# Optimization experiments

Measured on AMD Instinct MI355X. Metric: run time of the kernel, lower is better.

Reference implementation:

```python
import jax, jax.numpy as jnp
import numpy as np


def _binarize(x):
    # sign-binarization with straight-through estimator (matches torch .data trick)
    return x + jax.lax.stop_gradient(jnp.sign(x) - x)


def _conv(x, w):
    # x: NCHW, w: OIHW, stride 1, no padding (padding handled explicitly)
    return jax.lax.conv_general_dilated(
        x, w, window_strides=(1, 1), padding='VALID',
        dimension_numbers=('NCHW', 'OIHW', 'NCHW'))


def _hardtanh(x):
    return jnp.clip(x, -1.0, 1.0)


def _maxpool2(x):
    # 2x2 max pool, stride 2, over spatial dims of NCHW
    return jax.lax.reduce_window(
        x, -jnp.inf, jax.lax.max,
        window_dimensions=(1, 1, 2, 2), window_strides=(1, 1, 2, 2),
        padding='VALID')


def setup_inputs() -> dict:
    key = jax.random.key(0)
    kx, k1, k2, k3, k4 = jax.random.split(key, 5)
    x = jax.random.normal(kx, (32, 3, 512, 512), dtype=jnp.float32)
    w1 = jax.random.normal(k1, (8, 3, 3, 3), dtype=jnp.float32) * 0.1
    w2 = jax.random.normal(k2, (16, 8, 3, 3), dtype=jnp.float32) * 0.1
    w3 = jax.random.normal(k3, (32, 16, 3, 3), dtype=jnp.float32) * 0.1
    w4 = jax.random.normal(k4, (2, 32, 3, 3), dtype=jnp.float32) * 0.1
    return {'x': x, 'w1': w1, 'w2': w2, 'w3': w3, 'w4': w4}


def reference(x, w1, w2, w3, w4):
    # p0: ConstantPad2d(1, value=1)
    h = jnp.pad(x, ((0, 0), (0, 0), (1, 1), (1, 1)), constant_values=1.0)
    # features1: BinarizeConv2d(3,8) -- input has 3 channels so NOT binarized;
    # weights are sign-binarized. Then Hardtanh, MaxPool2d(2,2).
    h = _maxpool2(_hardtanh(_conv(h, _binarize(w1))))          # [B,8,256,256]
    # features2..4: binarize activations (C != 3) and weights, conv, hardtanh
    h = _hardtanh(_conv(_binarize(h), _binarize(w2)))          # [B,16,254,254]
    h = _hardtanh(_conv(_binarize(h), _binarize(w3)))          # [B,32,252,252]
    h = _hardtanh(_conv(_binarize(h), _binarize(w4)))          # [B,2,250,250]
    return h.reshape(h.shape[0], -1)                           # [B, 125000]
```

## Files before the change

### kernel.cpp

```cpp
#include <hip/hip_runtime.h>
#include <hip/hip_bf16.h>
#include <cstdint>


typedef __attribute__((ext_vector_type(2)))  float f32x2;
typedef __attribute__((ext_vector_type(4)))  int int4v;
typedef __attribute__((ext_vector_type(16))) int int16v;

#define WOFF_W2M 0
#define WOFF_W3M 10240
#define WOFF_W4P 20480
#define WOFF_W1D 28672
#define WEIGHTS_BYTES 32768

#define A1_PB (2*256*256*4)
#define A2_PB (4*254*254*4)

__device__ __forceinline__ int dot4(int a, int b, int c) {
#if __has_builtin(__builtin_amdgcn_sdot4)
    return __builtin_amdgcn_sdot4(a, b, c, false);
#else
    int s = c;
#pragma unroll
    for (int j = 0; j < 4; ++j) {
        int av = (a << (24 - 8 * j)) >> 24;
        int bv = (b << (24 - 8 * j)) >> 24;
        s += av * bv;
    }
    return s;
#endif
}

__device__ __forceinline__ int fsign(float w) {
    return (w > 0.f) ? 1 : ((w < 0.f) ? -1 : 0);
}

__device__ __forceinline__ void pkfma_lo(f32x2& acc, f32x2 w, f32x2 v) {
    asm("v_pk_fma_f32 %0, %1, %2, %0 op_sel:[0,0,0] op_sel_hi:[1,0,1]"
        : "+v"(acc) : "s"(w), "v"(v));
}
__device__ __forceinline__ void pkfma_hi(f32x2& acc, f32x2 w, f32x2 v) {
    asm("v_pk_fma_f32 %0, %1, %2, %0 op_sel:[0,1,0] op_sel_hi:[1,1,1]"
        : "+v"(acc) : "s"(w), "v"(v));
}

__global__ __launch_bounds__(256) void kprep(const float* __restrict__ w1,
                                             const float* __restrict__ w2,
                                             const float* __restrict__ w3,
                                             const float* __restrict__ w4,
                                             int* __restrict__ w2m,
                                             int* __restrict__ w3m,
                                             int* __restrict__ w4p,
                                             f32x2* __restrict__ w1d) {
    int tid = threadIdx.x;
    int b = blockIdx.x;
    if (b == 0) {
        for (int idx = tid; idx < 576; idx += 256) {
            int t = idx / 64, l = idx % 64;
            int oc = l & 31, icb = (l >> 5) * 16;
            int wd[4] = {0, 0, 0, 0};
            for (int j = 0; j < 16; ++j) {
                int ic = icb + j;
                int s = (oc < 16 && ic < 8) ? fsign(w2[(oc * 8 + ic) * 9 + t]) : 0;
                wd[j >> 2] |= (s & 0xff) << (8 * (j & 3));
            }
            w2m[idx * 4 + 0] = wd[0]; w2m[idx * 4 + 1] = wd[1];
            w2m[idx * 4 + 2] = wd[2]; w2m[idx * 4 + 3] = wd[3];
        }
    } else if (b == 1) {
        for (int idx = tid; idx < 576; idx += 256) {
            int t = idx / 64, l = idx % 64;
            int oc = l & 31, icb = (l >> 5) * 16;
            int wd[4] = {0, 0, 0, 0};
            for (int j = 0; j < 16; ++j) {
                int ic = icb + j;
                int s = (ic < 16) ? fsign(w3[(oc * 16 + ic) * 9 + t]) : 0;
                wd[j >> 2] |= (s & 0xff) << (8 * (j & 3));
            }
            w3m[idx * 4 + 0] = wd[0]; w3m[idx * 4 + 1] = wd[1];
            w3m[idx * 4 + 2] = wd[2]; w3m[idx * 4 + 3] = wd[3];
        }
    } else {
        for (int idx = tid; idx < 2 * 8 * 9; idx += 256) {
            int k = idx % 9, icg = (idx / 9) % 8, oc = idx / 72;
            int pack = 0;
#pragma unroll
            for (int j = 0; j < 4; ++j)
                pack |= (fsign(w4[(oc * 32 + icg * 4 + j) * 9 + k]) & 0xff) << (8 * j);
            w4p[idx] = pack;
        }
        for (int i = tid; i < 128; i += 256) {
            int op = i / 32, t = i % 32;
            f32x2 pr = {0.f, 0.f};
            if (t < 27) {
                float wa = w1[(2 * op) * 27 + t];
                float wbv = w1[(2 * op + 1) * 27 + t];
                pr[0] = (wa > 0.f) ? 1.f : ((wa < 0.f) ? -1.f : 0.f);
                pr[1] = (wbv > 0.f) ? 1.f : ((wbv < 0.f) ? -1.f : 0.f);
            }
            w1d[i] = pr;
        }
    }
}

__global__ __launch_bounds__(128, 4) void k1(const float* __restrict__ x,
                                             const f32x2* __restrict__ w1d,
                                             uint32_t* __restrict__ a1, int n0) {
    int tx = threadIdx.x;
    int oy = blockIdx.y;
    int ln = blockIdx.z;
    const float* xn = x + (size_t)(n0 + ln) * 3 * 512 * 512;

    int iy0 = 2 * oy - 1;
    int xb  = 4 * tx;

    f32x2 P[3][4][3];

    if (oy > 0 && oy < 255 && tx > 0 && tx < 127) {
#pragma unroll
        for (int ic = 0; ic < 3; ++ic) {
            const float* xc = xn + (size_t)ic * 512 * 512;
#pragma unroll
            for (int r = 0; r < 4; ++r) {
                const float* rp = xc + (size_t)(iy0 + r) * 512 + xb;
                float  lft = rp[-1];
                float4 m   = *(const float4*)rp;
                float  rgt = rp[4];
                P[ic][r][0] = (f32x2){lft, m.x};
                P[ic][r][1] = (f32x2){m.y, m.z};
                P[ic][r][2] = (f32x2){m.w, rgt};
            }
        }
    } else {
        for (int ic = 0; ic < 3; ++ic) {
            const float* xc = xn + (size_t)ic * 512 * 512;
#pragma unroll
            for (int r = 0; r < 4; ++r) {
                int iy = iy0 + r;
                bool yok = ((unsigned)iy < 512u);
                float t[6];
#pragma unroll
                for (int c = 0; c < 6; ++c) {
                    int ix = xb - 1 + c;
                    t[c] = (yok && ((unsigned)ix < 512u))
                               ? xc[(size_t)iy * 512 + ix] : 1.0f;
                }
                P[ic][r][0] = (f32x2){t[0], t[1]};
                P[ic][r][1] = (f32x2){t[2], t[3]};
                P[ic][r][2] = (f32x2){t[4], t[5]};
            }
        }
    }

#define PKTAP(ACC, ROW, COL)                                         \
    do {                                                             \
        if (((COL) & 1) == 0) pkfma_lo(ACC, ww, P[ic][ROW][(COL) >> 1]); \
        else                  pkfma_hi(ACC, ww, P[ic][ROW][(COL) >> 1]); \
    } while (0)

    uint64_t dallA = 0, dallB = 0;
#pragma unroll 1
    for (int op = 0; op < 4; ++op) {
        const f32x2* wb = w1d + op * 32;
        f32x2 wop[27];
#pragma unroll
        for (int t = 0; t < 27; ++t) wop[t] = wb[t];

        f32x2 aA00 = {0.f, 0.f}, aA01 = {0.f, 0.f};
        f32x2 aA10 = {0.f, 0.f}, aA11 = {0.f, 0.f};
        f32x2 aB00 = {0.f, 0.f}, aB01 = {0.f, 0.f};
        f32x2 aB10 = {0.f, 0.f}, aB11 = {0.f, 0.f};
#pragma unroll
        for (int ky = 0; ky < 3; ++ky) {
#pragma unroll
            for (int kx = 0; kx < 3; ++kx) {
#pragma unroll
                for (int ic = 0; ic < 3; ++ic) {
                    f32x2 ww = wop[ic * 9 + ky * 3 + kx];
                    PKTAP(aA00, ky + 0, kx + 0);
                    PKTAP(aA01, ky + 0, kx + 1);
                    PKTAP(aA10, ky + 1, kx + 0);
                    PKTAP(aA11, ky + 1, kx + 1);
                    PKTAP(aB00, ky + 0, kx + 2);
                    PKTAP(aB01, ky + 0, kx + 3);
                    PKTAP(aB10, ky + 1, kx + 2);
                    PKTAP(aB11, ky + 1, kx + 3);
                }
            }
        }
        float mA0 = fmaxf(fmaxf(aA00[0], aA01[0]), fmaxf(aA10[0], aA11[0]));
        float mA1 = fmaxf(fmaxf(aA00[1], aA01[1]), fmaxf(aA10[1], aA11[1]));
        float mB0 = fmaxf(fmaxf(aB00[0], aB01[0]), fmaxf(aB10[0], aB11[0]));
        float mB1 = fmaxf(fmaxf(aB00[1], aB01[1]), fmaxf(aB10[1], aB11[1]));
        int sA0 = (mA0 > 0.f) ? 1 : ((mA0 < 0.f) ? -1 : 0);
        int sA1 = (mA1 > 0.f) ? 1 : ((mA1 < 0.f) ? -1 : 0);
        int sB0 = (mB0 > 0.f) ? 1 : ((mB0 < 0.f) ? -1 : 0);
        int sB1 = (mB1 > 0.f) ? 1 : ((mB1 < 0.f) ? -1 : 0);
        dallA |= (uint64_t)(uint32_t)(sA0 & 0xff) << (8 * (2 * op));
        dallA |= (uint64_t)(uint32_t)(sA1 & 0xff) << (8 * (2 * op + 1));
        dallB |= (uint64_t)(uint32_t)(sB0 & 0xff) << (8 * (2 * op));
        dallB |= (uint64_t)(uint32_t)(sB1 & 0xff) << (8 * (2 * op + 1));
    }
#undef PKTAP

    size_t base = (((size_t)ln * 2) * 256 + oy) * 256 + 2 * tx;
    uint2 v0, v1;
    v0.x = (uint32_t)dallA;         v0.y = (uint32_t)dallB;
    v1.x = (uint32_t)(dallA >> 32); v1.y = (uint32_t)(dallB >> 32);
    *(uint2*)(a1 + base)             = v0;
    *(uint2*)(a1 + base + 256 * 256) = v1;
}

__global__ __launch_bounds__(256) void kconv2(const uint32_t* __restrict__ ain,
                                              const int* __restrict__ wm,
                                              uint32_t* __restrict__ aout) {
    __shared__ uint32_t stb[10][36][2];
    int w    = threadIdx.x >> 6;
    int lane = threadIdx.x & 63;
    int x0 = blockIdx.x * 32;
    int y0 = blockIdx.y * 8;
    int ln = blockIdx.z;

    const int4v* wmv = (const int4v*)wm;
    int4v bfr[9];
#pragma unroll
    for (int t = 0; t < 9; ++t) bfr[t] = wmv[t * 64 + lane];

    const uint32_t* abase = ain + (size_t)ln * 2 * 256 * 256;
    for (int idx = threadIdx.x; idx < 10 * 36 * 2; idx += 256) {
        int icg = idx & 1;
        int r2 = idx >> 1;
        int xx = r2 % 36, row = r2 / 36;
        int gy = y0 + row, gx = x0 + xx;
        uint32_t val = 0;
        if (xx < 34 && gx < 256 && gy < 256)
            val = abase[((size_t)icg * 256 + gy) * 256 + gx];
        stb[row][xx][icg] = val;
    }
    __syncthreads();

    int xl = lane & 31;
    int h  = lane >> 5;

#pragma unroll
    for (int ry = 0; ry < 2; ++ry) {
        int yy = y0 + 2 * w + ry;
        int16v acc = {};
#pragma unroll
        for (int ky = 0; ky < 3; ++ky) {
#pragma unroll
            for (int kx = 0; kx < 3; ++kx) {
                uint32_t d0 = stb[2 * w + ry + ky][xl + kx][0];
                uint32_t d1 = stb[2 * w + ry + ky][xl + kx][1];
                int4v a; a[0] = (int)d0; a[1] = (int)d1; a[2] = 0; a[3] = 0;
                acc = __builtin_amdgcn_mfma_i32_32x32x32_i8(bfr[ky * 3 + kx], a, acc, 0, 0, 0);
            }
        }
        bool ok = (yy < 254) && (x0 + xl < 254);
#pragma unroll
        for (int g = 0; g < 4; ++g) {
            int ocg = 2 * g + h;
            if (ocg < 4 && ok) {
                uint32_t dw = 0;
#pragma unroll
                for (int j = 0; j < 4; ++j) {
                    int v = min(max(acc[4 * g + j], -1), 1);
                    dw |= (uint32_t)(v & 0xff) << (8 * j);
                }
                aout[(((size_t)ln * 4 + ocg) * 254 + yy) * 254 + x0 + xl] = dw;
            }
        }
    }
}

__global__ __launch_bounds__(256) void kconv34(const uint32_t* __restrict__ a2,
                                               const int* __restrict__ w3m,
                                               const int* __restrict__ w4p,
                                               float* __restrict__ out, int n0) {
    __shared__ uint32_t sA2[12][68][4];
    __shared__ uint32_t sA3[10][8][64];
    int w    = threadIdx.x >> 6;
    int lane = threadIdx.x & 63;
    int x0 = blockIdx.x * 50;
    int y0 = blockIdx.y * 8;
    int ln = blockIdx.z;

    const int4v* wmv = (const int4v*)w3m;
    int4v bfr[9];
#pragma unroll
    for (int t = 0; t < 9; ++t) bfr[t] = wmv[t * 64 + lane];

    const uint32_t* abase = a2 + (size_t)ln * 4 * 254 * 254;
    for (int idx = threadIdx.x; idx < 12 * 66 * 4; idx += 256) {
        int icg = idx & 3;
        int r2 = idx >> 2;
        int xx = r2 % 66, row = r2 / 66;
        int gy = y0 + row, gx = x0 + xx;
        uint32_t val = 0;
        if (gy < 254 && gx < 254)
            val = abase[((size_t)icg * 254 + gy) * 254 + gx];
        sA2[row][xx][icg] = val;
    }
    __syncthreads();

    int xl = lane & 31;
    int h  = lane >> 5;
#pragma unroll
    for (int t5 = 0; t5 < 5; ++t5) {
        int t = w * 5 + t5;
        int ct = t / 10, row = t % 10;
        int16v acc = {};
#pragma unroll
        for (int ky = 0; ky < 3; ++ky) {
#pragma unroll
            for (int kx = 0; kx < 3; ++kx) {
                int4v a = *(const int4v*)&sA2[row + ky][ct * 32 + xl + kx][0];
                acc = __builtin_amdgcn_mfma_i32_32x32x32_i8(bfr[ky * 3 + kx], a, acc, 0, 0, 0);
            }
        }
#pragma unroll
        for (int g = 0; g < 4; ++g) {
            uint32_t dw = 0;
#pragma unroll
            for (int j = 0; j < 4; ++j) {
                int v = min(max(acc[4 * g + j], -1), 1);
                dw |= (uint32_t)(v & 0xff) << (8 * j);
            }
            sA3[row][2 * g + h][ct * 32 + xl] = dw;
        }
    }
    __syncthreads();

    size_t gn = (size_t)(n0 + ln);
    int o = threadIdx.x;
    if (o < 200) {
        int y  = o / 25;
        int xp = (o % 25) * 2;
        int gy = y0 + y;
        if (gy < 250) {
            int acc00 = 0, acc01 = 0, acc10 = 0, acc11 = 0;
#pragma unroll
            for (int icg = 0; icg < 8; ++icg) {
#pragma unroll
                for (int ky = 0; ky < 3; ++ky) {
                    uint2 lo = *(const uint2*)&sA3[y + ky][icg][xp];
                    uint2 hi = *(const uint2*)&sA3[y + ky][icg][xp + 2];
                    int c0 = (int)lo.x, c1 = (int)lo.y, c2 = (int)hi.x, c3 = (int)hi.y;
                    const int* wb0 = w4p + (0 * 8 + icg) * 9 + ky * 3;
                    const int* wb1 = w4p + (1 * 8 + icg) * 9 + ky * 3;
                    acc00 = dot4(c0, wb0[0], acc00);
                    acc00 = dot4(c1, wb0[1], acc00);
                    acc00 = dot4(c2, wb0[2], acc00);
                    acc01 = dot4(c0, wb1[0], acc01);
                    acc01 = dot4(c1, wb1[1], acc01);
                    acc01 = dot4(c2, wb1[2], acc01);
                    acc10 = dot4(c1, wb0[0], acc10);
                    acc10 = dot4(c2, wb0[1], acc10);
                    acc10 = dot4(c3, wb0[2], acc10);
                    acc11 = dot4(c1, wb1[0], acc11);
                    acc11 = dot4(c2, wb1[1], acc11);
                    acc11 = dot4(c3, wb1[2], acc11);
                }
            }
            float2 o0, o1;
            o0.x = fminf(fmaxf((float)acc00, -1.f), 1.f);
            o0.y = fminf(fmaxf((float)acc10, -1.f), 1.f);
            o1.x = fminf(fmaxf((float)acc01, -1.f), 1.f);
            o1.y = fminf(fmaxf((float)acc11, -1.f), 1.f);
            *(float2*)(out + ((gn * 2 + 0) * 250 + gy) * 250 + x0 + xp) = o0;
            *(float2*)(out + ((gn * 2 + 1) * 250 + gy) * 250 + x0 + xp) = o1;
        }
    }
}

extern "C" void kernel_launch(void* const* d_in, const int* in_sizes, int n_in,
                              void* d_out, int out_size, void* d_ws, size_t ws_size,
                              hipStream_t stream) {
    const float* x  = (const float*)d_in[0];
    const float* w1 = (const float*)d_in[1];
    const float* w2 = (const float*)d_in[2];
    const float* w3 = (const float*)d_in[3];
    const float* w4 = (const float*)d_in[4];
    char* ws = (char*)d_ws;

    int*   w2m = (int*)(ws + WOFF_W2M);
    int*   w3m = (int*)(ws + WOFF_W3M);
    int*   w4p = (int*)(ws + WOFF_W4P);
    f32x2* w1d = (f32x2*)(ws + WOFF_W1D);
    float* out = (float*)d_out;

    size_t per = (size_t)A1_PB + (size_t)A2_PB;
    int NC = 32;
    while (NC > 1 && (size_t)WEIGHTS_BYTES + (size_t)NC * per > ws_size) NC >>= 1;

    uint32_t* A1 = (uint32_t*)(ws + WEIGHTS_BYTES);
    uint32_t* A2 = (uint32_t*)(ws + WEIGHTS_BYTES + (size_t)NC * A1_PB);

    kprep<<<dim3(3), 256, 0, stream>>>(w1, w2, w3, w4, w2m, w3m, w4p, w1d);
    for (int n0 = 0; n0 < 32; n0 += NC) {
        k1<<<dim3(1, 256, NC), 128, 0, stream>>>(x, w1d, A1, n0);
        kconv2<<<dim3(8, 32, NC), 256, 0, stream>>>(A1, w2m, A2);
        kconv34<<<dim3(5, 32, NC), 256, 0, stream>>>(A2, w3m, w4p, out, n0);
    }
}
```

Before: 146.0 us.

## Compute conv4 with int8 MFMA and widen conv3/conv4 tile to 62 columns

Conv4 (32->2 channels) moves from per-thread sdot4 loops onto int8 32x32x32 MFMA. Its weights are packed into a padded 32-output matrix layout, and the conv3 output is stored in shared memory with a stride-9 interleaved layout so the MFMA B operand can be read directly. The block tile widens from 50 to 62 output columns, which reduces the number of tiles and the halo overhead. The cost is that MFMA computes 32 output channels when only 2 are needed, and B-operand loads are scalar-strided.

```diff
diff --git a/kernel.cpp b/kernel.cpp
--- a/kernel.cpp
+++ b/kernel.cpp
@@ -9,27 +9,12 @@
 
 #define WOFF_W2M 0
 #define WOFF_W3M 10240
-#define WOFF_W4P 20480
-#define WOFF_W1D 28672
+#define WOFF_W4M 20480
+#define WOFF_W1D 30720
 #define WEIGHTS_BYTES 32768
 
 #define A1_PB (2*256*256*4)
 #define A2_PB (4*254*254*4)
-
-__device__ __forceinline__ int dot4(int a, int b, int c) {
-#if __has_builtin(__builtin_amdgcn_sdot4)
-    return __builtin_amdgcn_sdot4(a, b, c, false);
-#else
-    int s = c;
-#pragma unroll
-    for (int j = 0; j < 4; ++j) {
-        int av = (a << (24 - 8 * j)) >> 24;
-        int bv = (b << (24 - 8 * j)) >> 24;
-        s += av * bv;
-    }
-    return s;
-#endif
-}
 
 __device__ __forceinline__ int fsign(float w) {
     return (w > 0.f) ? 1 : ((w < 0.f) ? -1 : 0);
@@ -50,7 +35,7 @@
                                              const float* __restrict__ w4,
                                              int* __restrict__ w2m,
                                              int* __restrict__ w3m,
-                                             int* __restrict__ w4p,
+                                             int* __restrict__ w4m,
                                              f32x2* __restrict__ w1d) {
     int tid = threadIdx.x;
     int b = blockIdx.x;
@@ -81,13 +66,17 @@
             w3m[idx * 4 + 2] = wd[2]; w3m[idx * 4 + 3] = wd[3];
         }
     } else {
-        for (int idx = tid; idx < 2 * 8 * 9; idx += 256) {
-            int k = idx % 9, icg = (idx / 9) % 8, oc = idx / 72;
-            int pack = 0;
-#pragma unroll
-            for (int j = 0; j < 4; ++j)
-                pack |= (fsign(w4[(oc * 32 + icg * 4 + j) * 9 + k]) & 0xff) << (8 * j);
-            w4p[idx] = pack;
+        for (int idx = tid; idx < 576; idx += 256) {
+            int t = idx / 64, l = idx % 64;
+            int oc = l & 31, icb = (l >> 5) * 16;
+            int wd[4] = {0, 0, 0, 0};
+            for (int j = 0; j < 16; ++j) {
+                int ic = icb + j;
+                int s = (oc < 2) ? fsign(w4[(oc * 32 + ic) * 9 + t]) : 0;
+                wd[j >> 2] |= (s & 0xff) << (8 * (j & 3));
+            }
+            w4m[idx * 4 + 0] = wd[0]; w4m[idx * 4 + 1] = wd[1];
+            w4m[idx * 4 + 2] = wd[2]; w4m[idx * 4 + 3] = wd[3];
         }
         for (int i = tid; i < 128; i += 256) {
             int op = i / 32, t = i % 32;
@@ -275,40 +264,50 @@
 
 __global__ __launch_bounds__(256) void kconv34(const uint32_t* __restrict__ a2,
                                                const int* __restrict__ w3m,
-                                               const int* __restrict__ w4p,
+                                               const int* __restrict__ w4m,
                                                float* __restrict__ out, int n0) {
     __shared__ uint32_t sA2[12][68][4];
-    __shared__ uint32_t sA3[10][8][64];
+    __shared__ uint32_t sA3[10 * 66 * 9];
     int w    = threadIdx.x >> 6;
     int lane = threadIdx.x & 63;
-    int x0 = blockIdx.x * 50;
+    int xl = lane & 31;
+    int h  = lane >> 5;
+    int x0 = blockIdx.x * 62;
     int y0 = blockIdx.y * 8;
     int ln = blockIdx.z;
 
-    const int4v* wmv = (const int4v*)w3m;
+    const int4v* wmv3 = (const int4v*)w3m;
     int4v bfr[9];
 #pragma unroll
-    for (int t = 0; t < 9; ++t) bfr[t] = wmv[t * 64 + lane];
+    for (int t = 0; t < 9; ++t) bfr[t] = wmv3[t * 64 + lane];
 
     const uint32_t* abase = a2 + (size_t)ln * 4 * 254 * 254;
-    for (int idx = threadIdx.x; idx < 12 * 66 * 4; idx += 256) {
+    for (int idx = threadIdx.x; idx < 12 * 64 * 4; idx += 256) {
+        int row = idx >> 8;
+        int xx  = (idx >> 2) & 63;
         int icg = idx & 3;
-        int r2 = idx >> 2;
-        int xx = r2 % 66, row = r2 / 66;
         int gy = y0 + row, gx = x0 + xx;
         uint32_t val = 0;
         if (gy < 254 && gx < 254)
             val = abase[((size_t)icg * 254 + gy) * 254 + gx];
         sA2[row][xx][icg] = val;
     }
+    if (threadIdx.x < 96) {
+        int row = threadIdx.x >> 3;
+        int xx  = 64 + ((threadIdx.x >> 2) & 1);
+        int icg = threadIdx.x & 3;
+        int gy = y0 + row, gx = x0 + xx;
+        uint32_t val = 0;
+        if (gy < 254 && gx < 254)
+            val = abase[((size_t)icg * 254 + gy) * 254 + gx];
+        sA2[row][xx][icg] = val;
+    }
     __syncthreads();
 
-    int xl = lane & 31;
-    int h  = lane >> 5;
 #pragma unroll
     for (int t5 = 0; t5 < 5; ++t5) {
-        int t = w * 5 + t5;
-        int ct = t / 10, row = t % 10;
+        int t = t5 * 4 + w;
+        int row = t >> 1, ct = t & 1;
         int16v acc = {};
 #pragma unroll
         for (int ky = 0; ky < 3; ++ky) {
@@ -318,6 +317,7 @@
                 acc = __builtin_amdgcn_mfma_i32_32x32x32_i8(bfr[ky * 3 + kx], a, acc, 0, 0, 0);
             }
         }
+        int pbase = (row * 66 + ct * 32 + xl) * 9;
 #pragma unroll
         for (int g = 0; g < 4; ++g) {
             uint32_t dw = 0;
@@ -326,49 +326,42 @@
                 int v = min(max(acc[4 * g + j], -1), 1);
                 dw |= (uint32_t)(v & 0xff) << (8 * j);
             }
-            sA3[row][2 * g + h][ct * 32 + xl] = dw;
-        }
-    }
+            sA3[pbase + 2 * g + h] = dw;
+        }
+    }
+
+    const int4v* wmv4 = (const int4v*)w4m;
+    int4v bf4[9];
+#pragma unroll
+    for (int t = 0; t < 9; ++t) bf4[t] = wmv4[t * 64 + lane];
     __syncthreads();
 
     size_t gn = (size_t)(n0 + ln);
-    int o = threadIdx.x;
-    if (o < 200) {
-        int y  = o / 25;
-        int xp = (o % 25) * 2;
+#pragma unroll
+    for (int t4 = 0; t4 < 4; ++t4) {
+        int t = t4 * 4 + w;
+        int y = t >> 1, ct2 = t & 1;
         int gy = y0 + y;
-        if (gy < 250) {
-            int acc00 = 0, acc01 = 0, acc10 = 0, acc11 = 0;
-#pragma unroll
-            for (int icg = 0; icg < 8; ++icg) {
-#pragma unroll
-                for (int ky = 0; ky < 3; ++ky) {
-                    uint2 lo = *(const uint2*)&sA3[y + ky][icg][xp];
-                    uint2 hi = *(const uint2*)&sA3[y + ky][icg][xp + 2];
-                    int c0 = (int)lo.x, c1 = (int)lo.y, c2 = (int)hi.x, c3 = (int)hi.y;
-                    const int* wb0 = w4p + (0 * 8 + icg) * 9 + ky * 3;
-                    const int* wb1 = w4p + (1 * 8 + icg) * 9 + ky * 3;
-                    acc00 = dot4(c0, wb0[0], acc00);
-                    acc00 = dot4(c1, wb0[1], acc00);
-                    acc00 = dot4(c2, wb0[2], acc00);
-                    acc01 = dot4(c0, wb1[0], acc01);
-                    acc01 = dot4(c1, wb1[1], acc01);
-                    acc01 = dot4(c2, wb1[2], acc01);
-                    acc10 = dot4(c1, wb0[0], acc10);
-                    acc10 = dot4(c2, wb0[1], acc10);
-                    acc10 = dot4(c3, wb0[2], acc10);
-                    acc11 = dot4(c1, wb1[0], acc11);
-                    acc11 = dot4(c2, wb1[1], acc11);
-                    acc11 = dot4(c3, wb1[2], acc11);
-                }
-            }
-            float2 o0, o1;
-            o0.x = fminf(fmaxf((float)acc00, -1.f), 1.f);
-            o0.y = fminf(fmaxf((float)acc10, -1.f), 1.f);
-            o1.x = fminf(fmaxf((float)acc01, -1.f), 1.f);
-            o1.y = fminf(fmaxf((float)acc11, -1.f), 1.f);
-            *(float2*)(out + ((gn * 2 + 0) * 250 + gy) * 250 + x0 + xp) = o0;
-            *(float2*)(out + ((gn * 2 + 1) * 250 + gy) * 250 + x0 + xp) = o1;
+        int16v acc = {};
+#pragma unroll
+        for (int ky = 0; ky < 3; ++ky) {
+#pragma unroll
+            for (int kx = 0; kx < 3; ++kx) {
+                const uint32_t* pb = &sA3[((y + ky) * 66 + ct2 * 32 + xl + kx) * 9 + h * 4];
+                int4v bv;
+                bv[0] = (int)pb[0]; bv[1] = (int)pb[1];
+                bv[2] = (int)pb[2]; bv[3] = (int)pb[3];
+                acc = __builtin_amdgcn_mfma_i32_32x32x32_i8(bf4[ky * 3 + kx], bv, acc, 0, 0, 0);
+            }
+        }
+        if (h == 0) {
+            int lx = ct2 * 32 + xl;
+            if (lx < 62 && x0 + lx < 250 && gy < 250) {
+                float v0 = fminf(fmaxf((float)acc[0], -1.f), 1.f);
+                float v1 = fminf(fmaxf((float)acc[1], -1.f), 1.f);
+                out[((gn * 2 + 0) * 250 + gy) * 250 + x0 + lx] = v0;
+                out[((gn * 2 + 1) * 250 + gy) * 250 + x0 + lx] = v1;
+            }
         }
     }
 }
@@ -385,7 +378,7 @@
 
     int*   w2m = (int*)(ws + WOFF_W2M);
     int*   w3m = (int*)(ws + WOFF_W3M);
-    int*   w4p = (int*)(ws + WOFF_W4P);
+    int*   w4m = (int*)(ws + WOFF_W4M);
     f32x2* w1d = (f32x2*)(ws + WOFF_W1D);
     float* out = (float*)d_out;
 
@@ -396,10 +389,10 @@
     uint32_t* A1 = (uint32_t*)(ws + WEIGHTS_BYTES);
     uint32_t* A2 = (uint32_t*)(ws + WEIGHTS_BYTES + (size_t)NC * A1_PB);
 
-    kprep<<<dim3(3), 256, 0, stream>>>(w1, w2, w3, w4, w2m, w3m, w4p, w1d);
+    kprep<<<dim3(3), 256, 0, stream>>>(w1, w2, w3, w4, w2m, w3m, w4m, w1d);
     for (int n0 = 0; n0 < 32; n0 += NC) {
         k1<<<dim3(1, 256, NC), 128, 0, stream>>>(x, w1d, A1, n0);
         kconv2<<<dim3(8, 32, NC), 256, 0, stream>>>(A1, w2m, A2);
-        kconv34<<<dim3(5, 32, NC), 256, 0, stream>>>(A2, w3m, w4p, out, n0);
-    }
-}
+        kconv34<<<dim3(5, 32, NC), 256, 0, stream>>>(A2, w3m, w4m, out, n0);
+    }
+}
```

After: 140.5 us. -3.8%, faster.
